# Kernel tuning notes

Measured on AMD Instinct MI355X. Metric: run time of the kernel, lower is better.

Reference implementation:

```python
import jax, jax.numpy as jnp
import numpy as np


def setup_inputs() -> dict:
    key = jax.random.key(0)
    k1, k2 = jax.random.split(key)
    B, G, N, C = 32, 64, 32, 3  # batch, num point groups, points per group, xyz
    xyz1_matrix = jax.random.normal(k1, (B, G, N, C), dtype=jnp.float32)
    xyz2_matrix = jax.random.normal(k2, (B, G, N, C), dtype=jnp.float32)
    return {"xyz1_matrix": xyz1_matrix, "xyz2_matrix": xyz2_matrix}


def reference(xyz1_matrix, xyz2_matrix):
    # xyz1_matrix: [B, G1, N1, 3], xyz2_matrix: [B, G2, N2, 3]
    # Pairwise squared L2 distances between every point of every group in set 1
    x2 = jnp.sum(xyz1_matrix * xyz1_matrix, axis=-1)  # [B, G1, N1]
    y2 = jnp.sum(xyz2_matrix * xyz2_matrix, axis=-1)  # [B, G2, N2]
    cross = jnp.einsum('bgnc,bhmc->bghnm', xyz1_matrix, xyz2_matrix)  # [B,G1,G2,N1,N2]
    d = x2[:, :, None, :, None] + y2[:, None, :, None, :] - 2.0 * cross
    # Nearest-neighbor (min over the other cloud) for both directions.
    dist1 = jnp.min(d, axis=-1)  # [B, G1, G2, N1]: for each pt in group g1, nearest in g2
    dist2 = jnp.min(d, axis=-2)  # [B, G1, G2, N2]: for each pt in group g2, nearest in g1
    # (dist2 here already corresponds to the torch dist2.permute(0, 2, 1, 3).)
    return jnp.mean(dist1, axis=-1) + jnp.mean(dist2, axis=-1)  # [B, G1, G2]
```

## Files before the change

### kernel.cpp

```cpp
#include <hip/hip_runtime.h>
#include <hip/hip_bf16.h>


__global__ __launch_bounds__(256, 2)
void chamfer_dist_kernel(const float* __restrict__ xyz1,
                         const float* __restrict__ xyz2,
                         float* __restrict__ out) {
    const int b    = blockIdx.x >> 4;
    const int g1   = ((blockIdx.x & 15) << 2) | (threadIdx.x >> 6);
    const int g2   = threadIdx.x & 63;

    const float* __restrict__ p2 = xyz2 + (size_t)(b * 64 + g2) * 96;
    float qx[32], qy[32], qz[32], s2[32];
#pragma unroll
    for (int m = 0; m < 32; ++m) {
        const float x = p2[3 * m + 0];
        const float y = p2[3 * m + 1];
        const float z = p2[3 * m + 2];
        s2[m] = fmaf(x, x, fmaf(y, y, z * z));
        qx[m] = -2.0f * x;
        qy[m] = -2.0f * y;
        qz[m] = -2.0f * z;
    }

    float colmin[32];
#pragma unroll
    for (int m = 0; m < 32; ++m) colmin[m] = 3.0e38f;

    const float* __restrict__ p1 = xyz1 + (size_t)(b * 64 + g1) * 96;
    float sum1 = 0.0f;

#pragma unroll 4
    for (int n = 0; n < 32; ++n) {
        const float x1 = p1[3 * n + 0];
        const float y1 = p1[3 * n + 1];
        const float z1 = p1[3 * n + 2];
        const float s1 = fmaf(x1, x1, fmaf(y1, y1, z1 * z1));
        float rmin = 3.0e38f;
#pragma unroll
        for (int m = 0; m < 32; ++m) {
            const float u = s1 + s2[m];
            const float t = fmaf(x1, qx[m], fmaf(y1, qy[m], fmaf(z1, qz[m], u)));
            rmin      = fminf(rmin, t);
            colmin[m] = fminf(colmin[m], t);
        }
        sum1 += rmin;
    }

    float sum2 = 0.0f;
#pragma unroll
    for (int m = 0; m < 32; ++m) sum2 += colmin[m];

    out[(size_t)(b * 64 + g1) * 64 + g2] = (sum1 + sum2) * (1.0f / 32.0f);
}

extern "C" void kernel_launch(void* const* d_in, const int* in_sizes, int n_in,
                              void* d_out, int out_size, void* d_ws, size_t ws_size,
                              hipStream_t stream) {
    const float* xyz1 = (const float*)d_in[0];
    const float* xyz2 = (const float*)d_in[1];
    float* out = (float*)d_out;

    dim3 grid(512);
    dim3 block(256);
    chamfer_dist_kernel<<<grid, block, 0, stream>>>(xyz1, xyz2, out);
}
```

Before: 73.15 us.

## Split each group pair across half-waves to double thread parallelism

Each output (g1,g2) is now computed by two lanes that each handle half of g2's points, with row minima and column sums combined via cross-half shuffles. Grid doubles and launch bounds allow 4 blocks per CU, reducing per-thread register arrays. xyz2 is loaded with float4 vector loads and the xyz1 base offset is made wave-uniform for scalar loads. Adds a shuffle per row iteration and redundant work on the xyz1 side.

```diff
diff --git a/kernel.cpp b/kernel.cpp
--- a/kernel.cpp
+++ b/kernel.cpp
@@ -1,33 +1,48 @@
 #include <hip/hip_runtime.h>
-#include <hip/hip_bf16.h>
 
 
-__global__ __launch_bounds__(256, 2)
+__global__ __launch_bounds__(256, 4)
 void chamfer_dist_kernel(const float* __restrict__ xyz1,
                          const float* __restrict__ xyz2,
                          float* __restrict__ out) {
-    const int b    = blockIdx.x >> 4;
-    const int g1   = ((blockIdx.x & 15) << 2) | (threadIdx.x >> 6);
-    const int g2   = threadIdx.x & 63;
+    const int b    = blockIdx.x >> 5;
+    const int pair = blockIdx.x & 31;
+    const int wave = threadIdx.x >> 6;
+    const int lane = threadIdx.x & 63;
+    const int g1   = (pair << 1) | (wave >> 1);
+    const int g2   = ((wave & 1) << 5) | (lane & 31);
+    const int half = lane >> 5;
 
-    const float* __restrict__ p2 = xyz2 + (size_t)(b * 64 + g2) * 96;
-    float qx[32], qy[32], qz[32], s2[32];
+    const float* __restrict__ p2 =
+        xyz2 + (size_t)(b * 64 + g2) * 96 + half * 48;
+    const float4* __restrict__ p2v = reinterpret_cast<const float4*>(p2);
+
+    float qx[16], qy[16], qz[16], s2[16], colmin[16];
 #pragma unroll
-    for (int m = 0; m < 32; ++m) {
-        const float x = p2[3 * m + 0];
-        const float y = p2[3 * m + 1];
-        const float z = p2[3 * m + 2];
-        s2[m] = fmaf(x, x, fmaf(y, y, z * z));
-        qx[m] = -2.0f * x;
-        qy[m] = -2.0f * y;
-        qz[m] = -2.0f * z;
+    for (int i = 0; i < 4; ++i) {
+        const float4 va = p2v[3 * i + 0];
+        const float4 vb = p2v[3 * i + 1];
+        const float4 vc = p2v[3 * i + 2];
+        const float f[12] = {va.x, va.y, va.z, va.w,
+                             vb.x, vb.y, vb.z, vb.w,
+                             vc.x, vc.y, vc.z, vc.w};
+#pragma unroll
+        for (int j = 0; j < 4; ++j) {
+            const int m = 4 * i + j;
+            const float x = f[3 * j + 0];
+            const float y = f[3 * j + 1];
+            const float z = f[3 * j + 2];
+            s2[m] = fmaf(x, x, fmaf(y, y, z * z));
+            qx[m] = -2.0f * x;
+            qy[m] = -2.0f * y;
+            qz[m] = -2.0f * z;
+            colmin[m] = 3.0e38f;
+        }
     }
 
-    float colmin[32];
-#pragma unroll
-    for (int m = 0; m < 32; ++m) colmin[m] = 3.0e38f;
+    const int off1 = __builtin_amdgcn_readfirstlane((b * 64 + g1) * 96);
+    const float* __restrict__ p1 = xyz1 + off1;
 
-    const float* __restrict__ p1 = xyz1 + (size_t)(b * 64 + g1) * 96;
     float sum1 = 0.0f;
 
 #pragma unroll 4
@@ -38,20 +53,28 @@
         const float s1 = fmaf(x1, x1, fmaf(y1, y1, z1 * z1));
         float rmin = 3.0e38f;
 #pragma unroll
-        for (int m = 0; m < 32; ++m) {
-            const float u = s1 + s2[m];
-            const float t = fmaf(x1, qx[m], fmaf(y1, qy[m], fmaf(z1, qz[m], u)));
-            rmin      = fminf(rmin, t);
-            colmin[m] = fminf(colmin[m], t);
+        for (int m = 0; m < 16; m += 2) {
+            const float t0 = fmaf(x1, qx[m],
+                             fmaf(y1, qy[m],
+                             fmaf(z1, qz[m], s1 + s2[m])));
+            const float t1 = fmaf(x1, qx[m + 1],
+                             fmaf(y1, qy[m + 1],
+                             fmaf(z1, qz[m + 1], s1 + s2[m + 1])));
+            rmin = fminf(fminf(t0, t1), rmin);
+            colmin[m]     = fminf(colmin[m], t0);
+            colmin[m + 1] = fminf(colmin[m + 1], t1);
         }
+        rmin = fminf(rmin, __shfl_xor(rmin, 32, 64));
         sum1 += rmin;
     }
 
     float sum2 = 0.0f;
 #pragma unroll
-    for (int m = 0; m < 32; ++m) sum2 += colmin[m];
+    for (int m = 0; m < 16; ++m) sum2 += colmin[m];
+    sum2 += __shfl_xor(sum2, 32, 64);
 
-    out[(size_t)(b * 64 + g1) * 64 + g2] = (sum1 + sum2) * (1.0f / 32.0f);
+    if (half == 0)
+        out[(size_t)(b * 64 + g1) * 64 + g2] = (sum1 + sum2) * (1.0f / 32.0f);
 }
 
 extern "C" void kernel_launch(void* const* d_in, const int* in_sizes, int n_in,
@@ -61,7 +84,7 @@
     const float* xyz2 = (const float*)d_in[1];
     float* out = (float*)d_out;
 
-    dim3 grid(512);
+    dim3 grid(1024);
     dim3 block(256);
     chamfer_dist_kernel<<<grid, block, 0, stream>>>(xyz1, xyz2, out);
 }
```

New measurement: 73.49 us. About the same (+0.5%).
